# Kernel tuning notes

Hardware: AMD Instinct MI355X
Metric: run time of the kernel (lower is better)

## Reference

```python
import jax, jax.numpy as jnp
import numpy as np

T, F_IN, UNITS, N_CLASSES = 21, 126, 8, 27


def _run_lstm(seq, Wk, Wr, b):
    """Keras-style LSTM (gate order i,f,g,o). seq: (B,T,F) -> hs: (B,T,U)."""
    B = seq.shape[0]
    U = Wr.shape[0]
    # input projection for all timesteps at once: (B,T,4U)
    z_in = jnp.einsum('btf,fg->btg', seq, Wk) + b

    def step(carry, z_t):
        h, c = carry
        z = z_t + h @ Wr
        i, f, g, o = jnp.split(z, 4, axis=-1)
        i = jax.nn.sigmoid(i)
        f = jax.nn.sigmoid(f)
        g = jnp.tanh(g)
        o = jax.nn.sigmoid(o)
        c = f * c + i * g
        h = o * jnp.tanh(c)
        return (h, c), h

    h0 = jnp.zeros((B, U), seq.dtype)
    (_, _), hs = jax.lax.scan(step, (h0, h0), jnp.swapaxes(z_in, 0, 1))
    return jnp.swapaxes(hs, 0, 1)  # (B,T,U)


def setup_inputs() -> dict:
    key = jax.random.key(0)
    ks = jax.random.split(key, 6)
    B = 32768
    return {
        'x': jax.random.normal(ks[0], (B, T * F_IN), dtype=jnp.float32),
        'W1k': jax.random.normal(ks[1], (F_IN, 4 * UNITS), dtype=jnp.float32) * 0.1,
        'W1r': jax.random.normal(ks[2], (UNITS, 4 * UNITS), dtype=jnp.float32) * 0.1,
        'b1': jnp.zeros((4 * UNITS,), jnp.float32),
        'W2k': jax.random.normal(ks[3], (UNITS, 4 * UNITS), dtype=jnp.float32) * 0.1,
        'W2r': jax.random.normal(ks[4], (UNITS, 4 * UNITS), dtype=jnp.float32) * 0.1,
        'b2': jnp.zeros((4 * UNITS,), jnp.float32),
        'Wd': jax.random.normal(ks[5], (UNITS, N_CLASSES), dtype=jnp.float32) * 0.1,
        'bd': jnp.zeros((N_CLASSES,), jnp.float32),
    }


def reference(x, W1k, W1r, b1, W2k, W2r, b2, Wd, bd):
    B = x.shape[0]
    seq = x.reshape(B, T, F_IN)            # Reshape((21, 126))
    h1 = _run_lstm(seq, W1k, W1r, b1)      # LSTM(8, return_sequences=True)
    # dropout is identity at inference
    h2 = _run_lstm(h1, W2k, W2r, b2)[:, -1]  # LSTM(8) -> last step (B,8)
    return jax.nn.softmax(h2 @ Wd + bd)    # Dense(27, softmax)
```

## Files before the change

### kernel.cpp

```cpp
#include <hip/hip_runtime.h>


namespace {
constexpr int T_  = 21;
constexpr int FIN = 126;
constexpr int U_  = 8;
constexpr int NC  = 27;
constexpr int ZC  = 4 * U_;
constexpr int ROW = T_ * FIN;
constexpr int NT  = 512;
constexpr int NPF = 8;
}

__device__ __forceinline__ float sigm(float x) {
  return __builtin_amdgcn_rcpf(1.0f + __expf(-x));
}
__device__ __forceinline__ float tanh_f(float x) {
  return 1.0f - 2.0f * __builtin_amdgcn_rcpf(1.0f + __expf(2.0f * x));
}

__global__ __launch_bounds__(NT, 4) void lstm_fused(
    const float* __restrict__ X,
    const float* __restrict__ W1k, const float* __restrict__ b1,
    const float* __restrict__ W1r,
    const float* __restrict__ W2k, const float* __restrict__ W2r,
    const float* __restrict__ b2,
    const float* __restrict__ Wd, const float* __restrict__ bd,
    float* __restrict__ out)
{
  __shared__ __align__(16) float wlds[FIN * ZC];
  __shared__ __align__(16) float xb[64 * FIN];
  __shared__ __align__(16) float zb1[ZC * 2 * 64];
  __shared__ __align__(16) float zb2[ZC * 2 * 64];

  const int tid = threadIdx.x;
  const int sl  = tid & 63;
  const int wv  = __builtin_amdgcn_readfirstlane(tid >> 6);
  const int cg  = wv & 3;
  const int fh  = wv >> 2;
  const int grp = blockIdx.x;

  int  goff[NPF];
  int  loff[NPF];
  bool val[NPF];
  #pragma unroll
  for (int k = 0; k < NPF; ++k) {
    int j = tid + k * NT;
    val[k] = (j < 64 * 63);
    int s = j / 63;
    int q = j - s * 63;
    goff[k] = s * ROW + 2 * q;
    loff[k] = s * FIN + 2 * q;
  }

  const float* xbase = X + (size_t)grp * 64 * ROW;

  const float*  Wrr = (fh == 0) ? W1r : W2r;
  const float4  b1a = reinterpret_cast<const float4*>(b1)[2 * cg];
  const float4  b1b = reinterpret_cast<const float4*>(b1)[2 * cg + 1];
  const float4  b2a = reinterpret_cast<const float4*>(b2)[2 * cg];
  const float4  b2b = reinterpret_cast<const float4*>(b2)[2 * cg + 1];

  float hs[U_], cs[U_];
  #pragma unroll
  for (int u = 0; u < U_; ++u) { hs[u] = 0.f; cs[u] = 0.f; }

  {
    const float2* w2 = reinterpret_cast<const float2*>(W1k);
    #pragma unroll
    for (int k = 0; k < 4; ++k) {
      int j = tid + k * NT;
      if (j < (FIN * ZC) / 2)
        reinterpret_cast<float2*>(wlds)[j] = w2[j];
    }
  }
  float2 pf[NPF];
  #pragma unroll
  for (int k = 0; k < NPF; ++k)
    if (val[k]) pf[k] = *reinterpret_cast<const float2*>(xbase + goff[k]);
  #pragma unroll
  for (int k = 0; k < NPF; ++k)
    if (val[k]) *reinterpret_cast<float2*>(&xb[loff[k]]) = pf[k];
  {
    const float* xt = xbase + FIN;
    #pragma unroll
    for (int k = 0; k < NPF; ++k)
      if (val[k]) pf[k] = *reinterpret_cast<const float2*>(xt + goff[k]);
  }
  __syncthreads();

  const float* wl = &wlds[8 * cg];
  const float* xr = &xb[sl * FIN];

  for (int t = 0; t < T_; ++t) {
    float4 za, zbv;
    if (fh == 0) { za = b1a; zbv = b1b; }
    else {
      za  = make_float4(0.f, 0.f, 0.f, 0.f);
      zbv = make_float4(0.f, 0.f, 0.f, 0.f);
    }

    auto run_gemm = [&](const int q0, const int qn) {
      #pragma unroll 4
      for (int qq = 0; qq < qn; ++qq) {
        const int q = q0 + qq;
        float2 xv  = *reinterpret_cast<const float2*>(&xr[2 * q]);
        float4 wa0 = *reinterpret_cast<const float4*>(&wl[(2 * q) * ZC]);
        float4 wb0 = *reinterpret_cast<const float4*>(&wl[(2 * q) * ZC + 4]);
        float4 wa1 = *reinterpret_cast<const float4*>(&wl[(2 * q + 1) * ZC]);
        float4 wb1 = *reinterpret_cast<const float4*>(&wl[(2 * q + 1) * ZC + 4]);
        za.x  = fmaf(xv.x, wa0.x, za.x);  za.y  = fmaf(xv.x, wa0.y, za.y);
        za.z  = fmaf(xv.x, wa0.z, za.z);  za.w  = fmaf(xv.x, wa0.w, za.w);
        zbv.x = fmaf(xv.x, wb0.x, zbv.x); zbv.y = fmaf(xv.x, wb0.y, zbv.y);
        zbv.z = fmaf(xv.x, wb0.z, zbv.z); zbv.w = fmaf(xv.x, wb0.w, zbv.w);
        za.x  = fmaf(xv.y, wa1.x, za.x);  za.y  = fmaf(xv.y, wa1.y, za.y);
        za.z  = fmaf(xv.y, wa1.z, za.z);  za.w  = fmaf(xv.y, wa1.w, za.w);
        zbv.x = fmaf(xv.y, wb1.x, zbv.x); zbv.y = fmaf(xv.y, wb1.y, zbv.y);
        zbv.z = fmaf(xv.y, wb1.z, zbv.z); zbv.w = fmaf(xv.y, wb1.w, zbv.w);
      }
    };
    if (fh == 0) run_gemm(0, 32);
    else         run_gemm(32, 31);

    if (fh == 0) {
      #pragma unroll
      for (int k = 0; k < U_; ++k) {
        float hv = hs[k];
        const float4* w = reinterpret_cast<const float4*>(&Wrr[k * ZC + 8 * cg]);
        float4 w0 = w[0], w1 = w[1];
        za.x  = fmaf(hv, w0.x, za.x);  za.y  = fmaf(hv, w0.y, za.y);
        za.z  = fmaf(hv, w0.z, za.z);  za.w  = fmaf(hv, w0.w, za.w);
        zbv.x = fmaf(hv, w1.x, zbv.x); zbv.y = fmaf(hv, w1.y, zbv.y);
        zbv.z = fmaf(hv, w1.z, zbv.z); zbv.w = fmaf(hv, w1.w, zbv.w);
      }
    }

    {
      float* zp = &zb1[(8 * cg) * 128 + fh * 64 + sl];
      zp[0 * 128] = za.x;  zp[1 * 128] = za.y;  zp[2 * 128] = za.z;  zp[3 * 128] = za.w;
      zp[4 * 128] = zbv.x; zp[5 * 128] = zbv.y; zp[6 * 128] = zbv.z; zp[7 * 128] = zbv.w;
    }
    __syncthreads();

    if (t + 1 < T_) {
      #pragma unroll
      for (int k = 0; k < NPF; ++k)
        if (val[k]) *reinterpret_cast<float2*>(&xb[loff[k]]) = pf[k];
    }
    if (t + 2 < T_) {
      const float* xt = xbase + (size_t)(t + 2) * FIN;
      #pragma unroll
      for (int k = 0; k < NPF; ++k)
        if (val[k]) pf[k] = *reinterpret_cast<const float2*>(xt + goff[k]);
    }

    if (fh == 0) {
      #pragma unroll
      for (int u = 0; u < U_; ++u) {
        const float* p0 = &zb1[u * 128 + sl];
        float zi = p0[0]        + p0[64];
        float zf = p0[ 8 * 128] + p0[ 8 * 128 + 64];
        float zg = p0[16 * 128] + p0[16 * 128 + 64];
        float zo = p0[24 * 128] + p0[24 * 128 + 64];
        float iv = sigm(zi), fv = sigm(zf), gv = tanh_f(zg), ov = sigm(zo);
        float cn = fv * cs[u] + iv * gv;
        cs[u] = cn;
        hs[u] = ov * tanh_f(cn);
      }
      float4 za2 = b2a, zb2v = b2b;
      #pragma unroll
      for (int k = 0; k < U_; ++k) {
        float hv = hs[k];
        const float4* w = reinterpret_cast<const float4*>(&W2k[k * ZC + 8 * cg]);
        float4 w0 = w[0], w1 = w[1];
        za2.x  = fmaf(hv, w0.x, za2.x);  za2.y  = fmaf(hv, w0.y, za2.y);
        za2.z  = fmaf(hv, w0.z, za2.z);  za2.w  = fmaf(hv, w0.w, za2.w);
        zb2v.x = fmaf(hv, w1.x, zb2v.x); zb2v.y = fmaf(hv, w1.y, zb2v.y);
        zb2v.z = fmaf(hv, w1.z, zb2v.z); zb2v.w = fmaf(hv, w1.w, zb2v.w);
      }
      float* zp = &zb2[(8 * cg) * 128 + 0 * 64 + sl];
      zp[0 * 128] = za2.x;  zp[1 * 128] = za2.y;  zp[2 * 128] = za2.z;  zp[3 * 128] = za2.w;
      zp[4 * 128] = zb2v.x; zp[5 * 128] = zb2v.y; zp[6 * 128] = zb2v.z; zp[7 * 128] = zb2v.w;
    } else {
      float4 za2  = make_float4(0.f, 0.f, 0.f, 0.f);
      float4 zb2v = make_float4(0.f, 0.f, 0.f, 0.f);
      #pragma unroll
      for (int k = 0; k < U_; ++k) {
        float hv = hs[k];
        const float4* w = reinterpret_cast<const float4*>(&Wrr[k * ZC + 8 * cg]);
        float4 w0 = w[0], w1 = w[1];
        za2.x  = fmaf(hv, w0.x, za2.x);  za2.y  = fmaf(hv, w0.y, za2.y);
        za2.z  = fmaf(hv, w0.z, za2.z);  za2.w  = fmaf(hv, w0.w, za2.w);
        zb2v.x = fmaf(hv, w1.x, zb2v.x); zb2v.y = fmaf(hv, w1.y, zb2v.y);
        zb2v.z = fmaf(hv, w1.z, zb2v.z); zb2v.w = fmaf(hv, w1.w, zb2v.w);
      }
      float* zp = &zb2[(8 * cg) * 128 + 1 * 64 + sl];
      zp[0 * 128] = za2.x;  zp[1 * 128] = za2.y;  zp[2 * 128] = za2.z;  zp[3 * 128] = za2.w;
      zp[4 * 128] = zb2v.x; zp[5 * 128] = zb2v.y; zp[6 * 128] = zb2v.z; zp[7 * 128] = zb2v.w;
    }
    __syncthreads();

    if (fh == 1) {
      #pragma unroll
      for (int u = 0; u < U_; ++u) {
        const float* p0 = &zb2[u * 128 + sl];
        float zi = p0[0]        + p0[64];
        float zf = p0[ 8 * 128] + p0[ 8 * 128 + 64];
        float zg = p0[16 * 128] + p0[16 * 128 + 64];
        float zo = p0[24 * 128] + p0[24 * 128 + 64];
        float iv = sigm(zi), fv = sigm(zf), gv = tanh_f(zg), ov = sigm(zo);
        float cn = fv * cs[u] + iv * gv;
        cs[u] = cn;
        hs[u] = ov * tanh_f(cn);
      }
    }
  }

  if (wv == 4) {
    float lg[NC];
    float m = -1e30f;
    #pragma unroll
    for (int c = 0; c < NC; ++c) {
      float acc = bd[c];
      #pragma unroll
      for (int k = 0; k < U_; ++k) acc = fmaf(hs[k], Wd[k * NC + c], acc);
      lg[c] = acc;
      m = fmaxf(m, acc);
    }
    float ssum = 0.f;
    #pragma unroll
    for (int c = 0; c < NC; ++c) {
      float e = __expf(lg[c] - m);
      lg[c] = e;
      ssum += e;
    }
    float inv = 1.0f / ssum;
    #pragma unroll
    for (int c = 0; c < NC; ++c) zb1[sl * NC + c] = lg[c] * inv;
  }
  __syncthreads();
  {
    float* oblk = out + (size_t)grp * 64 * NC;
    #pragma unroll
    for (int k = 0; k < 4; ++k) {
      int j = tid + k * NT;
      if (j < 64 * NC) oblk[j] = zb1[j];
    }
  }
}

extern "C" void kernel_launch(void* const* d_in, const int* in_sizes, int n_in,
                              void* d_out, int out_size, void* d_ws, size_t ws_size,
                              hipStream_t stream) {
  const float* X   = (const float*)d_in[0];
  const float* W1k = (const float*)d_in[1];
  const float* W1r = (const float*)d_in[2];
  const float* b1  = (const float*)d_in[3];
  const float* W2k = (const float*)d_in[4];
  const float* W2r = (const float*)d_in[5];
  const float* b2  = (const float*)d_in[6];
  const float* Wd  = (const float*)d_in[7];
  const float* bd  = (const float*)d_in[8];
  float* out = (float*)d_out;
  (void)d_ws; (void)ws_size;

  const int B    = in_sizes[0] / ROW;
  const int ngrp = B / 64;

  lstm_fused<<<dim3(ngrp), NT, 0, stream>>>(
      X, W1k, b1, W1r, W2k, W2r, b2, Wd, bd, out);
}
```

Measured before the change: 548.7 us.

## Stream input timesteps into LDS with async global_load_lds and restructure GEMM

Replaces the register-staged float2 prefetch of the next timestep's input with direct global-to-LDS async copies (global_load_lds, 4 bytes per lane), which frees the prefetch registers. The input-projection GEMM is rewritten as a software-pipelined, double-buffered loop over 4-feature chunks, with the weight and x buffers zero-padded to 128 features so both halves run 16 uniform chunks. Bias vectors are now reloaded from global memory instead of being held in registers. The risks are that the async LDS writes may race with reads without explicit waits, and that the copies now land only one step ahead instead of two, so less of the load latency is hidden.

```diff
diff --git a/kernel.cpp b/kernel.cpp
--- a/kernel.cpp
+++ b/kernel.cpp
@@ -9,7 +9,8 @@
 constexpr int ZC  = 4 * U_;
 constexpr int ROW = T_ * FIN;
 constexpr int NT  = 512;
-constexpr int NPF = 8;
+constexpr int NXD = 64 * FIN;
+constexpr int NLD = 16;
 }
 
 __device__ __forceinline__ float sigm(float x) {
@@ -18,6 +19,16 @@
 __device__ __forceinline__ float tanh_f(float x) {
   return 1.0f - 2.0f * __builtin_amdgcn_rcpf(1.0f + __expf(2.0f * x));
 }
+
+typedef unsigned int u32;
+__device__ __forceinline__ void async_cp4(const float* g, float* l) {
+  __builtin_amdgcn_global_load_lds(
+      (const __attribute__((address_space(1))) u32*)g,
+      (__attribute__((address_space(3))) u32*)l, 4, 0, 0);
+}
+
+struct WF { float4 a0, b0, a1, b1, a2, b2, a3, b3; };
+struct XF { float2 x01, x23; };
 
 __global__ __launch_bounds__(NT, 4) void lstm_fused(
     const float* __restrict__ X,
@@ -28,8 +39,8 @@
     const float* __restrict__ Wd, const float* __restrict__ bd,
     float* __restrict__ out)
 {
-  __shared__ __align__(16) float wlds[FIN * ZC];
-  __shared__ __align__(16) float xb[64 * FIN];
+  __shared__ __align__(16) float wlds[128 * ZC];
+  __shared__ __align__(16) float xb[NXD + 8];
   __shared__ __align__(16) float zb1[ZC * 2 * 64];
   __shared__ __align__(16) float zb2[ZC * 2 * 64];
 
@@ -40,26 +51,17 @@
   const int fh  = wv >> 2;
   const int grp = blockIdx.x;
 
-  int  goff[NPF];
-  int  loff[NPF];
-  bool val[NPF];
+  int soff[NLD];
   #pragma unroll
-  for (int k = 0; k < NPF; ++k) {
-    int j = tid + k * NT;
-    val[k] = (j < 64 * 63);
-    int s = j / 63;
-    int q = j - s * 63;
-    goff[k] = s * ROW + 2 * q;
-    loff[k] = s * FIN + 2 * q;
-  }
-
+  for (int k = 0; k < NLD; ++k) {
+    int d = tid + k * NT;
+    int s = d / FIN;
+    int f = d - s * FIN;
+    soff[k] = s * ROW + f;
+  }
   const float* xbase = X + (size_t)grp * 64 * ROW;
 
-  const float*  Wrr = (fh == 0) ? W1r : W2r;
-  const float4  b1a = reinterpret_cast<const float4*>(b1)[2 * cg];
-  const float4  b1b = reinterpret_cast<const float4*>(b1)[2 * cg + 1];
-  const float4  b2a = reinterpret_cast<const float4*>(b2)[2 * cg];
-  const float4  b2b = reinterpret_cast<const float4*>(b2)[2 * cg + 1];
+  const float* Wrr = (fh == 0) ? W1r : W2r;
 
   float hs[U_], cs[U_];
   #pragma unroll
@@ -70,57 +72,79 @@
     #pragma unroll
     for (int k = 0; k < 4; ++k) {
       int j = tid + k * NT;
-      if (j < (FIN * ZC) / 2)
-        reinterpret_cast<float2*>(wlds)[j] = w2[j];
-    }
-  }
-  float2 pf[NPF];
+      float2 v = make_float2(0.f, 0.f);
+      if (j < (FIN * ZC) / 2) v = w2[j];
+      reinterpret_cast<float2*>(wlds)[j] = v;
+    }
+    if (tid < 8) xb[NXD + tid] = 0.f;
+  }
   #pragma unroll
-  for (int k = 0; k < NPF; ++k)
-    if (val[k]) pf[k] = *reinterpret_cast<const float2*>(xbase + goff[k]);
-  #pragma unroll
-  for (int k = 0; k < NPF; ++k)
-    if (val[k]) *reinterpret_cast<float2*>(&xb[loff[k]]) = pf[k];
-  {
-    const float* xt = xbase + FIN;
-    #pragma unroll
-    for (int k = 0; k < NPF; ++k)
-      if (val[k]) pf[k] = *reinterpret_cast<const float2*>(xt + goff[k]);
+  for (int k = 0; k < NLD; ++k) {
+    if (k < 15 || wv < 6)
+      async_cp4(xbase + soff[k], &xb[k * NT + (wv << 6)]);
   }
   __syncthreads();
 
   const float* wl = &wlds[8 * cg];
   const float* xr = &xb[sl * FIN];
+  const int    fb = fh << 6;
 
   for (int t = 0; t < T_; ++t) {
     float4 za, zbv;
-    if (fh == 0) { za = b1a; zbv = b1b; }
-    else {
+    if (fh == 0) {
+      za  = reinterpret_cast<const float4*>(b1)[2 * cg];
+      zbv = reinterpret_cast<const float4*>(b1)[2 * cg + 1];
+    } else {
       za  = make_float4(0.f, 0.f, 0.f, 0.f);
       zbv = make_float4(0.f, 0.f, 0.f, 0.f);
     }
 
-    auto run_gemm = [&](const int q0, const int qn) {
-      #pragma unroll 4
-      for (int qq = 0; qq < qn; ++qq) {
-        const int q = q0 + qq;
-        float2 xv  = *reinterpret_cast<const float2*>(&xr[2 * q]);
-        float4 wa0 = *reinterpret_cast<const float4*>(&wl[(2 * q) * ZC]);
-        float4 wb0 = *reinterpret_cast<const float4*>(&wl[(2 * q) * ZC + 4]);
-        float4 wa1 = *reinterpret_cast<const float4*>(&wl[(2 * q + 1) * ZC]);
-        float4 wb1 = *reinterpret_cast<const float4*>(&wl[(2 * q + 1) * ZC + 4]);
-        za.x  = fmaf(xv.x, wa0.x, za.x);  za.y  = fmaf(xv.x, wa0.y, za.y);
-        za.z  = fmaf(xv.x, wa0.z, za.z);  za.w  = fmaf(xv.x, wa0.w, za.w);
-        zbv.x = fmaf(xv.x, wb0.x, zbv.x); zbv.y = fmaf(xv.x, wb0.y, zbv.y);
-        zbv.z = fmaf(xv.x, wb0.z, zbv.z); zbv.w = fmaf(xv.x, wb0.w, zbv.w);
-        za.x  = fmaf(xv.y, wa1.x, za.x);  za.y  = fmaf(xv.y, wa1.y, za.y);
-        za.z  = fmaf(xv.y, wa1.z, za.z);  za.w  = fmaf(xv.y, wa1.w, za.w);
-        zbv.x = fmaf(xv.y, wb1.x, zbv.x); zbv.y = fmaf(xv.y, wb1.y, zbv.y);
-        zbv.z = fmaf(xv.y, wb1.z, zbv.z); zbv.w = fmaf(xv.y, wb1.w, zbv.w);
-      }
+    auto ldw = [&](int c, WF& w) {
+      const float* p = wl + (fb + 4 * c) * ZC;
+      w.a0 = *reinterpret_cast<const float4*>(p);
+      w.b0 = *reinterpret_cast<const float4*>(p + 4);
+      w.a1 = *reinterpret_cast<const float4*>(p + ZC);
+      w.b1 = *reinterpret_cast<const float4*>(p + ZC + 4);
+      w.a2 = *reinterpret_cast<const float4*>(p + 2 * ZC);
+      w.b2 = *reinterpret_cast<const float4*>(p + 2 * ZC + 4);
+      w.a3 = *reinterpret_cast<const float4*>(p + 3 * ZC);
+      w.b3 = *reinterpret_cast<const float4*>(p + 3 * ZC + 4);
     };
-    if (fh == 0) run_gemm(0, 32);
-    else         run_gemm(32, 31);
+    auto ldx = [&](int c, XF& x) {
+      const float* p = xr + fb + 4 * c;
+      x.x01 = *reinterpret_cast<const float2*>(p);
+      x.x23 = *reinterpret_cast<const float2*>(p + 2);
+    };
+    auto dofma = [&](const WF& w, const XF& x) {
+      za.x  = fmaf(x.x01.x, w.a0.x, za.x);  za.y  = fmaf(x.x01.x, w.a0.y, za.y);
+      za.z  = fmaf(x.x01.x, w.a0.z, za.z);  za.w  = fmaf(x.x01.x, w.a0.w, za.w);
+      zbv.x = fmaf(x.x01.x, w.b0.x, zbv.x); zbv.y = fmaf(x.x01.x, w.b0.y, zbv.y);
+      zbv.z = fmaf(x.x01.x, w.b0.z, zbv.z); zbv.w = fmaf(x.x01.x, w.b0.w, zbv.w);
+      za.x  = fmaf(x.x01.y, w.a1.x, za.x);  za.y  = fmaf(x.x01.y, w.a1.y, za.y);
+      za.z  = fmaf(x.x01.y, w.a1.z, za.z);  za.w  = fmaf(x.x01.y, w.a1.w, za.w);
+      zbv.x = fmaf(x.x01.y, w.b1.x, zbv.x); zbv.y = fmaf(x.x01.y, w.b1.y, zbv.y);
+      zbv.z = fmaf(x.x01.y, w.b1.z, zbv.z); zbv.w = fmaf(x.x01.y, w.b1.w, zbv.w);
+      za.x  = fmaf(x.x23.x, w.a2.x, za.x);  za.y  = fmaf(x.x23.x, w.a2.y, za.y);
+      za.z  = fmaf(x.x23.x, w.a2.z, za.z);  za.w  = fmaf(x.x23.x, w.a2.w, za.w);
+      zbv.x = fmaf(x.x23.x, w.b2.x, zbv.x); zbv.y = fmaf(x.x23.x, w.b2.y, zbv.y);
+      zbv.z = fmaf(x.x23.x, w.b2.z, zbv.z); zbv.w = fmaf(x.x23.x, w.b2.w, zbv.w);
+      za.x  = fmaf(x.x23.y, w.a3.x, za.x);  za.y  = fmaf(x.x23.y, w.a3.y, za.y);
+      za.z  = fmaf(x.x23.y, w.a3.z, za.z);  za.w  = fmaf(x.x23.y, w.a3.w, za.w);
+      zbv.x = fmaf(x.x23.y, w.b3.x, zbv.x); zbv.y = fmaf(x.x23.y, w.b3.y, zbv.y);
+      zbv.z = fmaf(x.x23.y, w.b3.z, zbv.z); zbv.w = fmaf(x.x23.y, w.b3.w, zbv.w);
+    };
+
+    {
+      WF wA, wB; XF xA, xB;
+      ldw(0, wA); ldx(0, xA);
+      #pragma unroll
+      for (int cc = 0; cc < 8; ++cc) {
+        ldw(2 * cc + 1, wB); ldx(2 * cc + 1, xB);
+        dofma(wA, xA);
+        if (cc < 7) { ldw(2 * cc + 2, wA); ldx(2 * cc + 2, xA); }
+        dofma(wB, xB);
+      }
+    }
 
     if (fh == 0) {
       #pragma unroll
@@ -143,15 +167,12 @@
     __syncthreads();
 
     if (t + 1 < T_) {
-      #pragma unroll
-      for (int k = 0; k < NPF; ++k)
-        if (val[k]) *reinterpret_cast<float2*>(&xb[loff[k]]) = pf[k];
-    }
-    if (t + 2 < T_) {
-      const float* xt = xbase + (size_t)(t + 2) * FIN;
-      #pragma unroll
-      for (int k = 0; k < NPF; ++k)
-        if (val[k]) pf[k] = *reinterpret_cast<const float2*>(xt + goff[k]);
+      const float* xt = xbase + (size_t)(t + 1) * FIN;
+      #pragma unroll
+      for (int k = 0; k < NLD; ++k) {
+        if (k < 15 || wv < 6)
+          async_cp4(xt + soff[k], &xb[k * NT + (wv << 6)]);
+      }
     }
 
     if (fh == 0) {
@@ -167,7 +188,8 @@
         cs[u] = cn;
         hs[u] = ov * tanh_f(cn);
       }
-      float4 za2 = b2a, zb2v = b2b;
+      float4 za2 = reinterpret_cast<const float4*>(b2)[2 * cg];
+      float4 zb2v = reinterpret_cast<const float4*>(b2)[2 * cg + 1];
       #pragma unroll
       for (int k = 0; k < U_; ++k) {
         float hv = hs[k];
```

Result: slower. 917.8 us (+67.3%).

## Stream LSTM input weights through scalar loads instead of LDS

Applied to the files above, without the earlier changes.

Removes the LDS copy of the 126x32 input-projection weight matrix. Each wave, whose column group is wave-uniform, instead fetches its weights every timestep with inline-asm s_load_dwordx8 into SGPRs and uses them as scalar FMA operands. Bias loads also move inside the loop to relieve VGPR pressure. This cuts LDS read traffic and LDS footprint, in exchange for heavy SGPR use, a full lgkmcnt(0) wait per group, and scalar-cache reloads on every step.

```diff
diff --git a/kernel.cpp b/kernel.cpp
--- a/kernel.cpp
+++ b/kernel.cpp
@@ -19,6 +19,95 @@
   return 1.0f - 2.0f * __builtin_amdgcn_rcpf(1.0f + __expf(2.0f * x));
 }
 
+typedef __attribute__((ext_vector_type(8))) float f32x8;
+
+struct SW8 { f32x8 r0, r1, r2, r3, r4, r5, r6, r7; };
+struct SW6 { f32x8 r0, r1, r2, r3, r4, r5; };
+
+template<int G>
+__device__ __forceinline__ void sload8(SW8& A, const float* wkp) {
+  asm volatile(
+      "s_load_dwordx8 %0, %8, %9\n\t"
+      "s_load_dwordx8 %1, %8, %10\n\t"
+      "s_load_dwordx8 %2, %8, %11\n\t"
+      "s_load_dwordx8 %3, %8, %12\n\t"
+      "s_load_dwordx8 %4, %8, %13\n\t"
+      "s_load_dwordx8 %5, %8, %14\n\t"
+      "s_load_dwordx8 %6, %8, %15\n\t"
+      "s_load_dwordx8 %7, %8, %16"
+      : "=s"(A.r0), "=s"(A.r1), "=s"(A.r2), "=s"(A.r3),
+        "=s"(A.r4), "=s"(A.r5), "=s"(A.r6), "=s"(A.r7)
+      : "s"(wkp),
+        "i"(G * 1024 + 0),   "i"(G * 1024 + 128),
+        "i"(G * 1024 + 256), "i"(G * 1024 + 384),
+        "i"(G * 1024 + 512), "i"(G * 1024 + 640),
+        "i"(G * 1024 + 768), "i"(G * 1024 + 896));
+}
+
+__device__ __forceinline__ void sload6(SW6& A, const float* wkp) {
+  asm volatile(
+      "s_load_dwordx8 %0, %6, %7\n\t"
+      "s_load_dwordx8 %1, %6, %8\n\t"
+      "s_load_dwordx8 %2, %6, %9\n\t"
+      "s_load_dwordx8 %3, %6, %10\n\t"
+      "s_load_dwordx8 %4, %6, %11\n\t"
+      "s_load_dwordx8 %5, %6, %12"
+      : "=s"(A.r0), "=s"(A.r1), "=s"(A.r2), "=s"(A.r3),
+        "=s"(A.r4), "=s"(A.r5)
+      : "s"(wkp),
+        "i"(56 * 128), "i"(57 * 128), "i"(58 * 128),
+        "i"(59 * 128), "i"(60 * 128), "i"(61 * 128));
+}
+
+__device__ __forceinline__ void swait8(SW8& A, float2& x0, float2& x1,
+                                       float2& x2, float2& x3) {
+  asm volatile("s_waitcnt lgkmcnt(0)"
+               : "+s"(A.r0), "+s"(A.r1), "+s"(A.r2), "+s"(A.r3),
+                 "+s"(A.r4), "+s"(A.r5), "+s"(A.r6), "+s"(A.r7),
+                 "+v"(x0), "+v"(x1), "+v"(x2), "+v"(x3));
+}
+__device__ __forceinline__ void swait6(SW6& A, float2& x0, float2& x1,
+                                       float2& x2) {
+  asm volatile("s_waitcnt lgkmcnt(0)"
+               : "+s"(A.r0), "+s"(A.r1), "+s"(A.r2), "+s"(A.r3),
+                 "+s"(A.r4), "+s"(A.r5),
+                 "+v"(x0), "+v"(x1), "+v"(x2));
+}
+
+__device__ __forceinline__ void fma_row(float* acc, float xv, const f32x8& w) {
+  #pragma unroll
+  for (int c = 0; c < 8; ++c) acc[c] = fmaf(xv, w[c], acc[c]);
+}
+
+template<int NG, int TROWS, int G = 0>
+__device__ __forceinline__ void gemm_groups(const float* wkp, const float* xh,
+                                            float* acc) {
+  if constexpr (G < NG) {
+    SW8 A;
+    sload8<G>(A, wkp);
+    float2 x0 = *reinterpret_cast<const float2*>(xh + 8 * G + 0);
+    float2 x1 = *reinterpret_cast<const float2*>(xh + 8 * G + 2);
+    float2 x2 = *reinterpret_cast<const float2*>(xh + 8 * G + 4);
+    float2 x3 = *reinterpret_cast<const float2*>(xh + 8 * G + 6);
+    swait8(A, x0, x1, x2, x3);
+    fma_row(acc, x0.x, A.r0); fma_row(acc, x0.y, A.r1);
+    fma_row(acc, x1.x, A.r2); fma_row(acc, x1.y, A.r3);
+    fma_row(acc, x2.x, A.r4); fma_row(acc, x2.y, A.r5);
+    fma_row(acc, x3.x, A.r6); fma_row(acc, x3.y, A.r7);
+    gemm_groups<NG, TROWS, G + 1>(wkp, xh, acc);
+  } else if constexpr (TROWS == 6) {
+    SW6 A;
+    sload6(A, wkp);
+    float2 x0 = *reinterpret_cast<const float2*>(xh + 8 * G + 0);
+    float2 x1 = *reinterpret_cast<const float2*>(xh + 8 * G + 2);
+    float2 x2 = *reinterpret_cast<const float2*>(xh + 8 * G + 4);
+    swait6(A, x0, x1, x2);
+    fma_row(acc, x0.x, A.r0); fma_row(acc, x0.y, A.r1);
+    fma_row(acc, x1.x, A.r2); fma_row(acc, x1.y, A.r3);
+    fma_row(acc, x2.x, A.r4); fma_row(acc, x2.y, A.r5);
+  }
+}
+
 __global__ __launch_bounds__(NT, 4) void lstm_fused(
     const float* __restrict__ X,
     const float* __restrict__ W1k, const float* __restrict__ b1,
@@ -28,7 +117,6 @@
     const float* __restrict__ Wd, const float* __restrict__ bd,
     float* __restrict__ out)
 {
-  __shared__ __align__(16) float wlds[FIN * ZC];
   __shared__ __align__(16) float xb[64 * FIN];
   __shared__ __align__(16) float zb1[ZC * 2 * 64];
   __shared__ __align__(16) float zb2[ZC * 2 * 64];
@@ -55,25 +143,13 @@
 
   const float* xbase = X + (size_t)grp * 64 * ROW;
 
-  const float*  Wrr = (fh == 0) ? W1r : W2r;
-  const float4  b1a = reinterpret_cast<const float4*>(b1)[2 * cg];
-  const float4  b1b = reinterpret_cast<const float4*>(b1)[2 * cg + 1];
-  const float4  b2a = reinterpret_cast<const float4*>(b2)[2 * cg];
-  const float4  b2b = reinterpret_cast<const float4*>(b2)[2 * cg + 1];
+  const float* wkp = W1k + (fh ? 64 * ZC : 0) + 8 * cg;
+  const float* Wrr = (fh == 0) ? W1r : W2r;
 
   float hs[U_], cs[U_];
   #pragma unroll
   for (int u = 0; u < U_; ++u) { hs[u] = 0.f; cs[u] = 0.f; }
 
-  {
-    const float2* w2 = reinterpret_cast<const float2*>(W1k);
-    #pragma unroll
-    for (int k = 0; k < 4; ++k) {
-      int j = tid + k * NT;
-      if (j < (FIN * ZC) / 2)
-        reinterpret_cast<float2*>(wlds)[j] = w2[j];
-    }
-  }
   float2 pf[NPF];
   #pragma unroll
   for (int k = 0; k < NPF; ++k)
@@ -89,38 +165,22 @@
   }
   __syncthreads();
 
-  const float* wl = &wlds[8 * cg];
   const float* xr = &xb[sl * FIN];
 
   for (int t = 0; t < T_; ++t) {
-    float4 za, zbv;
-    if (fh == 0) { za = b1a; zbv = b1b; }
-    else {
-      za  = make_float4(0.f, 0.f, 0.f, 0.f);
-      zbv = make_float4(0.f, 0.f, 0.f, 0.f);
-    }
-
-    auto run_gemm = [&](const int q0, const int qn) {
-      #pragma unroll 4
-      for (int qq = 0; qq < qn; ++qq) {
-        const int q = q0 + qq;
-        float2 xv  = *reinterpret_cast<const float2*>(&xr[2 * q]);
-        float4 wa0 = *reinterpret_cast<const float4*>(&wl[(2 * q) * ZC]);
-        float4 wb0 = *reinterpret_cast<const float4*>(&wl[(2 * q) * ZC + 4]);
-        float4 wa1 = *reinterpret_cast<const float4*>(&wl[(2 * q + 1) * ZC]);
-        float4 wb1 = *reinterpret_cast<const float4*>(&wl[(2 * q + 1) * ZC + 4]);
-        za.x  = fmaf(xv.x, wa0.x, za.x);  za.y  = fmaf(xv.x, wa0.y, za.y);
-        za.z  = fmaf(xv.x, wa0.z, za.z);  za.w  = fmaf(xv.x, wa0.w, za.w);
-        zbv.x = fmaf(xv.x, wb0.x, zbv.x); zbv.y = fmaf(xv.x, wb0.y, zbv.y);
-        zbv.z = fmaf(xv.x, wb0.z, zbv.z); zbv.w = fmaf(xv.x, wb0.w, zbv.w);
-        za.x  = fmaf(xv.y, wa1.x, za.x);  za.y  = fmaf(xv.y, wa1.y, za.y);
-        za.z  = fmaf(xv.y, wa1.z, za.z);  za.w  = fmaf(xv.y, wa1.w, za.w);
-        zbv.x = fmaf(xv.y, wb1.x, zbv.x); zbv.y = fmaf(xv.y, wb1.y, zbv.y);
-        zbv.z = fmaf(xv.y, wb1.z, zbv.z); zbv.w = fmaf(xv.y, wb1.w, zbv.w);
-      }
-    };
-    if (fh == 0) run_gemm(0, 32);
-    else         run_gemm(32, 31);
+    float acc[8];
+    if (fh == 0) {
+      float4 ba = reinterpret_cast<const float4*>(b1)[2 * cg];
+      float4 bb = reinterpret_cast<const float4*>(b1)[2 * cg + 1];
+      acc[0] = ba.x; acc[1] = ba.y; acc[2] = ba.z; acc[3] = ba.w;
+      acc[4] = bb.x; acc[5] = bb.y; acc[6] = bb.z; acc[7] = bb.w;
+    } else {
+      #pragma unroll
+      for (int c = 0; c < 8; ++c) acc[c] = 0.f;
+    }
+
+    if (fh == 0) gemm_groups<8, 0>(wkp, xr, acc);
+    else         gemm_groups<7, 6>(wkp, xr + 64, acc);
 
     if (fh == 0) {
       #pragma unroll
@@ -128,17 +188,17 @@
         float hv = hs[k];
         const float4* w = reinterpret_cast<const float4*>(&Wrr[k * ZC + 8 * cg]);
         float4 w0 = w[0], w1 = w[1];
-        za.x  = fmaf(hv, w0.x, za.x);  za.y  = fmaf(hv, w0.y, za.y);
-        za.z  = fmaf(hv, w0.z, za.z);  za.w  = fmaf(hv, w0.w, za.w);
-        zbv.x = fmaf(hv, w1.x, zbv.x); zbv.y = fmaf(hv, w1.y, zbv.y);
-        zbv.z = fmaf(hv, w1.z, zbv.z); zbv.w = fmaf(hv, w1.w, zbv.w);
+        acc[0] = fmaf(hv, w0.x, acc[0]); acc[1] = fmaf(hv, w0.y, acc[1]);
+        acc[2] = fmaf(hv, w0.z, acc[2]); acc[3] = fmaf(hv, w0.w, acc[3]);
+        acc[4] = fmaf(hv, w1.x, acc[4]); acc[5] = fmaf(hv, w1.y, acc[5]);
+        acc[6] = fmaf(hv, w1.z, acc[6]); acc[7] = fmaf(hv, w1.w, acc[7]);
       }
     }
 
     {
       float* zp = &zb1[(8 * cg) * 128 + fh * 64 + sl];
-      zp[0 * 128] = za.x;  zp[1 * 128] = za.y;  zp[2 * 128] = za.z;  zp[3 * 128] = za.w;
-      zp[4 * 128] = zbv.x; zp[5 * 128] = zbv.y; zp[6 * 128] = zbv.z; zp[7 * 128] = zbv.w;
+      #pragma unroll
+      for (int c = 0; c < 8; ++c) zp[c * 128] = acc[c];
     }
     __syncthreads();
 
@@ -167,7 +227,8 @@
         cs[u] = cn;
         hs[u] = ov * tanh_f(cn);
       }
-      float4 za2 = b2a, zb2v = b2b;
+      float4 za2  = reinterpret_cast<const float4*>(b2)[2 * cg];
+      float4 zb2v = reinterpret_cast<const float4*>(b2)[2 * cg + 1];
       #pragma unroll
       for (int k = 0; k < U_; ++k) {
         float hv = hs[k];
```

Result: faster. 515.4 us (-6.1%).
